# Optimization experiments

Hardware: AMD Instinct MI355X
Metric: run time of the kernel (lower is better)

The kernel has to match this reference:

```python
import jax, jax.numpy as jnp
import numpy as np

B, N, T, F = 4, 256, 16, 128
H = 256

def setup_inputs() -> dict:
    key = jax.random.key(0)
    k1, k2, k3, k4, k5 = jax.random.split(key, 5)
    bound1 = 1.0 / np.sqrt(2 * F)
    bound2 = 1.0 / np.sqrt(H)
    return {
        "nodefeat": jax.random.normal(k1, (B, N, T, F), dtype=jnp.float32),
        "W1": jax.random.uniform(k2, (H, 2 * F), minval=-bound1, maxval=bound1, dtype=jnp.float32),
        "b1": jax.random.uniform(k3, (H,), minval=-bound1, maxval=bound1, dtype=jnp.float32),
        "W2": jax.random.uniform(k4, (1, H), minval=-bound2, maxval=bound2, dtype=jnp.float32),
        "b2": jax.random.uniform(k5, (1,), minval=-bound2, maxval=bound2, dtype=jnp.float32),
    }

def reference(nodefeat, W1, b1, W2, b2):
    # nodefeat: [B,N,T,F] -> mean over time -> h: [B,N,F]
    h = jnp.mean(nodefeat, axis=2)
    f = h.shape[-1]
    # Split W1 to avoid materializing the [B,N,N,2F] concat:
    # Linear(cat(h_i,h_j)) = h_i @ W1[:, :F].T + h_j @ W1[:, F:].T + b1
    a = jnp.einsum('bnf,hf->bnh', h, W1[:, :f])  # contribution of h_i
    c = jnp.einsum('bnf,hf->bnh', h, W1[:, f:])  # contribution of h_j
    pre = a[:, :, None, :] + c[:, None, :, :] + b1  # [B,N,N,H]
    act = jax.nn.relu(pre)
    logits = jnp.einsum('bijh,h->bij', act, W2[0]) + b2[0]  # [B,N,N]
    return logits
```

## Files before the change

### kernel.cpp

```cpp
#include <hip/hip_runtime.h>

#define B_ 4
#define N_ 256
#define T_ 16
#define F_ 128
#define H_ 256
#define BN_ (B_ * N_)

__global__ __launch_bounds__(1024) void lp_prep(const float* __restrict__ nf,
                                                const float* __restrict__ W1,
                                                float* __restrict__ hbar,
                                                float* __restrict__ W1T) {
    __shared__ float sT[64][65];
    const int tid = threadIdx.x;
    if (blockIdx.x < 128) {
        const int idx = blockIdx.x * 1024 + tid;
        const int bn  = idx >> 7;
        const int f   = idx & 127;
        const float* src = nf + (size_t)bn * (T_ * F_) + f;
        float s = 0.f;
#pragma unroll
        for (int t = 0; t < T_; ++t) s += src[t * F_];
        hbar[idx] = s * (1.0f / 16.0f);
    } else {
        const int t  = blockIdx.x - 128;
        const int y0 = (t >> 2) * 64;
        const int x0 = (t & 3) * 64;
        const int ty = tid >> 6;
        const int tx = tid & 63;
#pragma unroll
        for (int r = 0; r < 4; ++r)
            sT[r * 16 + ty][tx] = W1[(size_t)(y0 + r * 16 + ty) * 256 + (x0 + tx)];
        __syncthreads();
#pragma unroll
        for (int r = 0; r < 4; ++r)
            W1T[(size_t)(x0 + r * 16 + ty) * 256 + (y0 + tx)] = sT[tx][r * 16 + ty];
    }
}

__global__ __launch_bounds__(512) void lp_gemm(const float* __restrict__ hbar,
                                               const float* __restrict__ W1T,
                                               const float* __restrict__ b1,
                                               float* __restrict__ aT,
                                               float* __restrict__ cT) {
    __shared__ float red[16][4][128];

    const int tile8 = blockIdx.x >> 1;
    const int h0    = (blockIdx.x & 1) * 128;
    const int bn0   = tile8 * 8;
    const int b     = bn0 >> 8;
    const int tid   = threadIdx.x;
    const int kq    = __builtin_amdgcn_readfirstlane(tid >> 7);
    const int hl    = tid & 127;
    const int h     = h0 + hl;

    const float* wA = W1T + (size_t)(kq * 32) * H_ + h;
    const float* wC = W1T + (size_t)(F_ + kq * 32) * H_ + h;
    const float* hb = hbar + (size_t)bn0 * F_ + kq * 32;

    float acca[8] = {0.f, 0.f, 0.f, 0.f, 0.f, 0.f, 0.f, 0.f};
    float accc[8] = {0.f, 0.f, 0.f, 0.f, 0.f, 0.f, 0.f, 0.f};

#pragma unroll 4
    for (int kk = 0; kk < 32; ++kk) {
        const float wa = wA[(size_t)kk * H_];
        const float wc = wC[(size_t)kk * H_];
#pragma unroll
        for (int n = 0; n < 8; ++n) {
            const float hv = hb[n * F_ + kk];
            acca[n] = fmaf(hv, wa, acca[n]);
            accc[n] = fmaf(hv, wc, accc[n]);
        }
    }

#pragma unroll
    for (int n = 0; n < 8; ++n) {
        red[n][kq][hl]     = acca[n];
        red[8 + n][kq][hl] = accc[n];
    }
    __syncthreads();

    const int rv = tid >> 7;
#pragma unroll
    for (int i = 0; i < 4; ++i) {
        const int v = rv * 4 + i;
        const float s = (red[v][0][hl] + red[v][1][hl]) + (red[v][2][hl] + red[v][3][hl]);
        if (v < 8) {
            const int bn = bn0 + v;
            aT[((size_t)(bn >> 2) * H_ + h) * 4 + (bn & 3)] = s + b1[h];
        } else {
            const int n = v - 8;
            cT[((size_t)b * H_ + h) * N_ + ((bn0 & 255) + n)] = s;
        }
    }
}

__global__ __launch_bounds__(1024) void lp_k2(const float* __restrict__ aT,
                                              const float* __restrict__ cT,
                                              const float* __restrict__ W2,
                                              const float* __restrict__ b2,
                                              float* __restrict__ out) {
    __shared__ float pr[4][4][256];

    const int tile = blockIdx.x;
    const int bn0  = tile * 4;
    const int b    = bn0 >> 8;
    const int i0   = bn0 & 255;
    const int tid  = threadIdx.x;
    const int hq   = __builtin_amdgcn_readfirstlane(tid >> 8);
    const int j    = tid & 255;

    const float* crow = cT + (size_t)b * (H_ * N_) + j;
    const float* arow = aT + (size_t)tile * (H_ * 4);
    const int h0 = hq * 64;

    float acc0 = 0.f, acc1 = 0.f, acc2 = 0.f, acc3 = 0.f;

#pragma unroll 8
    for (int hh = 0; hh < 64; ++hh) {
        const int h = h0 + hh;
        const float cj = crow[(size_t)h * N_];
        const float w  = W2[h];
        const float4 av = *(const float4*)(arow + h * 4);
        float x;
        x = av.x + cj; acc0 = fmaf(fmaxf(x, 0.f), w, acc0);
        x = av.y + cj; acc1 = fmaf(fmaxf(x, 0.f), w, acc1);
        x = av.z + cj; acc2 = fmaf(fmaxf(x, 0.f), w, acc2);
        x = av.w + cj; acc3 = fmaf(fmaxf(x, 0.f), w, acc3);
    }

    pr[0][hq][j] = acc0;
    pr[1][hq][j] = acc1;
    pr[2][hq][j] = acc2;
    pr[3][hq][j] = acc3;
    __syncthreads();

    const int r  = tid >> 8;
    const int jj = tid & 255;
    const float s = (pr[r][0][jj] + pr[r][1][jj]) + (pr[r][2][jj] + pr[r][3][jj]);
    out[((size_t)b * N_ + (i0 + r)) * N_ + jj] = s + b2[0];
}

extern "C" void kernel_launch(void* const* d_in, const int* in_sizes, int n_in,
                              void* d_out, int out_size, void* d_ws, size_t ws_size,
                              hipStream_t stream) {
    const float* nodefeat = (const float*)d_in[0];
    const float* W1       = (const float*)d_in[1];
    const float* b1       = (const float*)d_in[2];
    const float* W2       = (const float*)d_in[3];
    const float* b2       = (const float*)d_in[4];
    float* out = (float*)d_out;

    float* hbar = (float*)d_ws;
    float* W1T  = hbar + (size_t)BN_ * F_;
    float* aT   = W1T + 256 * 256;
    float* cT   = aT + (size_t)256 * H_ * 4;

    lp_prep<<<144, 1024, 0, stream>>>(nodefeat, W1, hbar, W1T);
    lp_gemm<<<256, 512, 0, stream>>>(hbar, W1T, b1, aT, cT);
    lp_k2<<<256, 1024, 0, stream>>>(aT, cT, W2, b2, out);
}
```

Before: 25.69 us.

## Retile pairwise kernel to 2 rows x 4 columns per thread with float4 loads

The pairwise relu-dot kernel now gives each thread 2 i-rows by 4 j-columns over 32 hidden units, loading c with float4 and a with float2. The grid goes from 256 blocks of 1024 threads to 512 blocks of 512 threads, and the partial sums are reduced across 8 hidden-dimension slices in shared memory. The aim is more register reuse per load and fewer load instructions per FMA. The cost is a longer shared-memory reduction and a different occupancy and latency profile.

```diff
diff --git a/kernel.cpp b/kernel.cpp
--- a/kernel.cpp
+++ b/kernel.cpp
@@ -95,50 +95,55 @@
     }
 }
 
-__global__ __launch_bounds__(1024) void lp_k2(const float* __restrict__ aT,
-                                              const float* __restrict__ cT,
-                                              const float* __restrict__ W2,
-                                              const float* __restrict__ b2,
-                                              float* __restrict__ out) {
-    __shared__ float pr[4][4][256];
+__global__ __launch_bounds__(512) void lp_k2(const float* __restrict__ aT,
+                                             const float* __restrict__ cT,
+                                             const float* __restrict__ W2,
+                                             const float* __restrict__ b2,
+                                             float* __restrict__ out) {
+    __shared__ float pr[8][2][256];
 
-    const int tile = blockIdx.x;
-    const int bn0  = tile * 4;
-    const int b    = bn0 >> 8;
-    const int i0   = bn0 & 255;
-    const int tid  = threadIdx.x;
-    const int hq   = __builtin_amdgcn_readfirstlane(tid >> 8);
-    const int j    = tid & 255;
+    const int blk = blockIdx.x;
+    const int bn0 = blk * 2;
+    const int b   = bn0 >> 8;
+    const int tid = threadIdx.x;
+    const int ho  = __builtin_amdgcn_readfirstlane(tid >> 6);
+    const int jq  = tid & 63;
+    const int j0  = jq * 4;
 
-    const float* crow = cT + (size_t)b * (H_ * N_) + j;
-    const float* arow = aT + (size_t)tile * (H_ * 4);
-    const int h0 = hq * 64;
+    const float* crow  = cT + (size_t)b * (H_ * N_) + j0;
+    const float* abase = aT + ((size_t)(bn0 >> 2) * H_) * 4 + (bn0 & 3);
+    const int h0 = ho * 32;
 
-    float acc0 = 0.f, acc1 = 0.f, acc2 = 0.f, acc3 = 0.f;
+    float a00 = 0.f, a01 = 0.f, a02 = 0.f, a03 = 0.f;
+    float a10 = 0.f, a11 = 0.f, a12 = 0.f, a13 = 0.f;
 
 #pragma unroll 8
-    for (int hh = 0; hh < 64; ++hh) {
+    for (int hh = 0; hh < 32; ++hh) {
         const int h = h0 + hh;
-        const float cj = crow[(size_t)h * N_];
-        const float w  = W2[h];
-        const float4 av = *(const float4*)(arow + h * 4);
+        const float4 cj = *(const float4*)(crow + (size_t)h * N_);
+        const float  w  = W2[h];
+        const float2 a2 = *(const float2*)(abase + h * 4);
         float x;
-        x = av.x + cj; acc0 = fmaf(fmaxf(x, 0.f), w, acc0);
-        x = av.y + cj; acc1 = fmaf(fmaxf(x, 0.f), w, acc1);
-        x = av.z + cj; acc2 = fmaf(fmaxf(x, 0.f), w, acc2);
-        x = av.w + cj; acc3 = fmaf(fmaxf(x, 0.f), w, acc3);
+        x = a2.x + cj.x; a00 = fmaf(fmaxf(x, 0.f), w, a00);
+        x = a2.x + cj.y; a01 = fmaf(fmaxf(x, 0.f), w, a01);
+        x = a2.x + cj.z; a02 = fmaf(fmaxf(x, 0.f), w, a02);
+        x = a2.x + cj.w; a03 = fmaf(fmaxf(x, 0.f), w, a03);
+        x = a2.y + cj.x; a10 = fmaf(fmaxf(x, 0.f), w, a10);
+        x = a2.y + cj.y; a11 = fmaf(fmaxf(x, 0.f), w, a11);
+        x = a2.y + cj.z; a12 = fmaf(fmaxf(x, 0.f), w, a12);
+        x = a2.y + cj.w; a13 = fmaf(fmaxf(x, 0.f), w, a13);
     }
 
-    pr[0][hq][j] = acc0;
-    pr[1][hq][j] = acc1;
-    pr[2][hq][j] = acc2;
-    pr[3][hq][j] = acc3;
+    *(float4*)(&pr[ho][0][j0]) = make_float4(a00, a01, a02, a03);
+    *(float4*)(&pr[ho][1][j0]) = make_float4(a10, a11, a12, a13);
     __syncthreads();
 
-    const int r  = tid >> 8;
-    const int jj = tid & 255;
-    const float s = (pr[r][0][jj] + pr[r][1][jj]) + (pr[r][2][jj] + pr[r][3][jj]);
-    out[((size_t)b * N_ + (i0 + r)) * N_ + jj] = s + b2[0];
+    const int r2 = tid >> 8;
+    const int j  = tid & 255;
+    float s = 0.f;
+#pragma unroll
+    for (int o = 0; o < 8; ++o) s += pr[o][r2][j];
+    out[(size_t)(bn0 + r2) * N_ + j] = s + b2[0];
 }
 
 extern "C" void kernel_launch(void* const* d_in, const int* in_sizes, int n_in,
@@ -158,5 +163,5 @@
 
     lp_prep<<<144, 1024, 0, stream>>>(nodefeat, W1, hbar, W1T);
     lp_gemm<<<256, 512, 0, stream>>>(hbar, W1T, b1, aT, cT);
-    lp_k2<<<256, 1024, 0, stream>>>(aT, cT, W2, b2, out);
+    lp_k2<<<512, 512, 0, stream>>>(aT, cT, W2, b2, out);
 }
```

After: 31.14 us. 1.21x slower.
